# Optimization experiments

Hardware: AMD Instinct MI355X
Metric: run time of the kernel (lower is better)

The kernel has to match this reference:

```python
import jax, jax.numpy as jnp
import numpy as np

B, C_IN, H, W = 4, 1536, 64, 64   # SGI input: cat of three 512-ch encoder maps at 64x64
HID, OUT = 1536, 512
N = H * W


def _grid_edge_index(h, w):
    # 4-connected bidirectional grid, matching SGI.grid_edge_index
    idx = np.arange(h * w).reshape(h, w)
    right = np.stack([idx[:, :-1].ravel(), idx[:, 1:].ravel()])
    down = np.stack([idx[:-1, :].ravel(), idx[1:, :].ravel()])
    ei = np.concatenate([right, down, right[::-1], down[::-1]], axis=1)
    return ei.astype(np.int32)


def setup_inputs() -> dict:
    key = jax.random.key(0)
    ks = jax.random.split(key, 7)
    ei = _grid_edge_index(H, W)
    s = 0.02
    return {
        "x":  jax.random.normal(ks[0], (B, C_IN, H, W), jnp.float32),
        "W1": jax.random.normal(ks[1], (C_IN, HID), jnp.float32) * s,
        "b1": jnp.zeros((HID,), jnp.float32),
        "W2": jax.random.normal(ks[2], (HID, OUT), jnp.float32) * s,
        "b2": jnp.zeros((OUT,), jnp.float32),
        "Wl": jax.random.normal(ks[3], (C_IN, OUT), jnp.float32) * s,
        "bl": jnp.zeros((OUT,), jnp.float32),
        "src": jnp.asarray(ei[0]),
        "dst": jnp.asarray(ei[1]),
    }


def _gcn(h_in, Wt, b, src, dst, inv_sqrt_deg, inv_deg):
    # PyG GCNConv: lin -> symmetric-normalized aggregation (with self loops) -> +bias
    h = h_in @ Wt                                   # [B, N, F]
    norm = inv_sqrt_deg[src] * inv_sqrt_deg[dst]    # [E]
    msgs = h[:, src, :] * norm[None, :, None]       # [B, E, F]
    # self-loop contribution has norm 1/deg_i
    agg = (h * inv_deg[None, :, None]).at[:, dst, :].add(msgs)
    return agg + b


def reference(x, W1, b1, W2, b2, Wl, bl, src, dst):
    Bb, C, Hh, Ww = x.shape
    n = Hh * Ww
    # degree including self loop (graph is symmetric)
    deg = jnp.zeros((n,), x.dtype).at[dst].add(1.0) + 1.0
    inv_sqrt_deg = jax.lax.rsqrt(deg)
    inv_deg = 1.0 / deg

    xt = x.reshape(Bb, C, n).transpose(0, 2, 1)     # [B, N, C]
    identity = xt
    origin = xt @ Wl + bl                           # [B, N, OUT]
    h = jax.nn.relu(_gcn(xt, W1, b1, src, dst, inv_sqrt_deg, inv_deg))
    h = _gcn(h + identity, W2, b2, src, dst, inv_sqrt_deg, inv_deg)
    out = h * origin                                # [B, N, OUT]
    return out.transpose(0, 2, 1).reshape(Bb, out.shape[-1], Hh, Ww)
```

## Files before the change

### kernel.cpp

```cpp
#include <hip/hip_runtime.h>
#include <hip/hip_bf16.h>
#include <stdint.h>


typedef __bf16 bf16;
typedef float f32x4 __attribute__((ext_vector_type(4)));
typedef bf16 bf16x8 __attribute__((ext_vector_type(8)));

#define NB 4
#define NN 4096
#define CIN 1536
#define HIDF 1536
#define OUTF 512

__device__ __forceinline__ float degree_of(int n) {
  const int x = n & 63, y = n >> 6;
  return 1.0f + (x > 0) + (x < 63) + (y > 0) + (y < 63);
}
__device__ __forceinline__ float deg2(int gx, int gy) {
  return 1.0f + (gx > 0) + (gx < 63) + (gy > 0) + (gy < 63);
}

#define XBLK 6144
#define W1BLK 576
#define W2BLK 192

__global__ __launch_bounds__(256) void prep(
    const float* __restrict__ x, const float* __restrict__ W1,
    const float* __restrict__ W2, const float* __restrict__ Wl,
    bf16* __restrict__ xt, bf16* __restrict__ xa, bf16* __restrict__ w1t,
    bf16* __restrict__ w2t, bf16* __restrict__ wlt) {
  __shared__ float vt[64 * 64];
  __shared__ float at[64 * 64];
  const int B = blockIdx.x, t = threadIdx.x;
  const int tx = t & 15, ty = t >> 4;
  const int lane = t & 63, w = t >> 6;
  const int u = lane & 7, n3 = lane >> 3;

  if (B < XBLK) {
    const int slot = B >> 3;
    const int nt = (B & 7) * 8 + (slot & 7);
    const int ct = (slot >> 3) % 24;
    const int bb = (slot >> 3) / 24;
    const int gy = nt;
    const int n0 = nt * 64, c0 = ct * 64;
    const float* xb = x + (long)bb * CIN * NN;
#pragma unroll
    for (int cc = 0; cc < 4; cc++) {
      const int cl = ty * 4 + cc;
      const float* row = xb + (long)(c0 + cl) * NN + n0;
      const int nb = tx * 4;
      f32x4 v = *(const f32x4*)(row + nb);
      f32x4 up = {0.f, 0.f, 0.f, 0.f};
      f32x4 dn = {0.f, 0.f, 0.f, 0.f};
      if (gy > 0) up = *(const f32x4*)(row + nb - 64);
      if (gy < 63) dn = *(const f32x4*)(row + nb + 64);
      const float lf = (tx > 0) ? row[nb - 1] : 0.f;
      const float rt = (tx < 15) ? row[nb + 4] : 0.f;
      f32x4 a;
#pragma unroll
      for (int i = 0; i < 4; i++) {
        const int gx = nb + i;
        const float degn = deg2(gx, gy);
        float s = v[i] * (1.0f / degn);
        const float lv = (i == 0) ? lf : v[i - 1];
        const float rv = (i == 3) ? rt : v[i + 1];
        if (gx > 0) s += lv * rsqrtf(degn * deg2(gx - 1, gy));
        if (gx < 63) s += rv * rsqrtf(degn * deg2(gx + 1, gy));
        if (gy > 0) s += up[i] * rsqrtf(degn * deg2(gx, gy - 1));
        if (gy < 63) s += dn[i] * rsqrtf(degn * deg2(gx, gy + 1));
        a[i] = s;
      }
      const int chunk = tx ^ (2 * ((cl >> 3) & 7));
      *(f32x4*)&vt[cl * 64 + chunk * 4] = v;
      *(f32x4*)&at[cl * 64 + chunk * 4] = a;
    }
    __syncthreads();
    bf16* xtb = xt + (long)bb * NN * CIN;
    bf16* xab = xa + (long)bb * NN * CIN;
#pragma unroll
    for (int q = 0; q < 4; q++) {
      const int j = q * 4 + w;
      const int arr = j & 1, r = j >> 1;
      const int nl = n3 + 8 * r;
      const float* s = arr ? at : vt;
      bf16x8 o;
#pragma unroll
      for (int jj = 0; jj < 8; jj++) {
        const int cl = u * 8 + jj;
        const int col = nl ^ (8 * ((cl >> 3) & 7));
        o[jj] = (bf16)s[cl * 64 + col];
      }
      bf16* outp = arr ? xab : xtb;
      *(bf16x8*)&outp[(long)(n0 + nl) * CIN + c0 + u * 8] = o;
    }
  } else {
    int B2 = B - XBLK;
    const float* srcp;
    bf16* dstp;
    int Fdim, Kd, nt, ct;
    if (B2 < W1BLK) {
      nt = B2 / 24; ct = B2 % 24; srcp = W1; dstp = w1t; Fdim = HIDF; Kd = CIN;
    } else if (B2 < W1BLK + W2BLK) {
      const int l = B2 - W1BLK;
      nt = l / 24; ct = l % 24; srcp = W2; dstp = w2t; Fdim = OUTF; Kd = HIDF;
    } else {
      const int l = B2 - W1BLK - W2BLK;
      nt = l / 24; ct = l % 24; srcp = Wl; dstp = wlt; Fdim = OUTF; Kd = CIN;
    }
    const int n0 = nt * 64, c0 = ct * 64;
#pragma unroll
    for (int cc = 0; cc < 4; cc++) {
      const int cl = ty * 4 + cc;
      const float* row = srcp + (long)(c0 + cl) * Fdim + n0;
      f32x4 v = *(const f32x4*)(row + tx * 4);
      const int chunk = tx ^ (2 * ((cl >> 3) & 7));
      *(f32x4*)&vt[cl * 64 + chunk * 4] = v;
    }
    __syncthreads();
#pragma unroll
    for (int q = 0; q < 2; q++) {
      const int r = q * 4 + w;
      const int nl = n3 + 8 * r;
      bf16x8 o;
#pragma unroll
      for (int jj = 0; jj < 8; jj++) {
        const int cl = u * 8 + jj;
        const int col = nl ^ (8 * ((cl >> 3) & 7));
        o[jj] = (bf16)vt[cl * 64 + col];
      }
      *(bf16x8*)&dstp[(long)(n0 + nl) * Kd + c0 + u * 8] = o;
    }
  }
}

__device__ __forceinline__ void async_copy16(const void* g, void* l) {
  __builtin_amdgcn_global_load_lds(
      (const __attribute__((address_space(1))) void*)g,
      (__attribute__((address_space(3))) void*)l, 16, 0, 0);
}

struct GemmCtx {
  f32x4 acc[4][4];
  int wave, lane, wm, wn, quad, l15;
};

__device__ __forceinline__ void gemm_init(GemmCtx& cx, int t) {
  cx.wave = t >> 6;
  cx.lane = t & 63;
  cx.wm = (cx.wave & 1) * 64;
  cx.wn = (cx.wave >> 1) * 64;
  cx.quad = cx.lane >> 4;
  cx.l15 = cx.lane & 15;
#pragma unroll
  for (int i = 0; i < 4; i++)
#pragma unroll
    for (int j = 0; j < 4; j++) cx.acc[i][j] = {0.f, 0.f, 0.f, 0.f};
}

template <int K>
__device__ __forceinline__ void gemm_kloop(GemmCtx& cx, const bf16* Ab,
                                           const bf16* Bb, bf16* As,
                                           bf16* Bs) {
  const int r = cx.lane >> 3, c8 = cx.lane & 7;
  const int fchunk = c8 ^ r;
  constexpr int NT = K / 64;
#pragma unroll
  for (int i = 0; i < 4; i++) {
    const int row = i * 32 + cx.wave * 8;
    async_copy16(Ab + (long)(row + r) * K + fchunk * 8, &As[row * 64]);
    async_copy16(Bb + (long)(row + r) * K + fchunk * 8, &Bs[row * 64]);
  }
  __syncthreads();
#pragma unroll 2
  for (int t = 0; t < NT; ++t) {
    const int cur = (t & 1) * (128 * 64);
    const int nxt = cur ^ (128 * 64);
    const int ktn = ((t + 1 < NT) ? t + 1 : t) * 64;
#pragma unroll
    for (int i = 0; i < 4; i++) {
      const int row = i * 32 + cx.wave * 8;
      async_copy16(Ab + (long)(row + r) * K + ktn + fchunk * 8,
                   &As[nxt + row * 64]);
      async_copy16(Bb + (long)(row + r) * K + ktn + fchunk * 8,
                   &Bs[nxt + row * 64]);
    }
#pragma unroll
    for (int kk = 0; kk < 2; kk++) {
      const int q = kk * 4 + cx.quad;
      bf16x8 af[4], bfv[4];
#pragma unroll
      for (int mr = 0; mr < 4; mr++) {
        const int m = cx.wm + mr * 16 + cx.l15;
        af[mr] = *(const bf16x8*)&As[cur + m * 64 + (q ^ (m & 7)) * 8];
      }
#pragma unroll
      for (int nc = 0; nc < 4; nc++) {
        const int n = cx.wn + nc * 16 + cx.l15;
        bfv[nc] = *(const bf16x8*)&Bs[cur + n * 64 + (q ^ (n & 7)) * 8];
      }
#pragma unroll
      for (int mr = 0; mr < 4; mr++)
#pragma unroll
        for (int nc = 0; nc < 4; nc++)
          cx.acc[mr][nc] = __builtin_amdgcn_mfma_f32_16x16x32_bf16(
              af[mr], bfv[nc], cx.acc[mr][nc], 0, 0, 0);
    }
    __syncthreads();
  }
}

__global__ __launch_bounds__(256) void gemm_h(
    const bf16* __restrict__ xa, const bf16* __restrict__ w1t,
    const bf16* __restrict__ xt, bf16* __restrict__ h,
    const float* __restrict__ b1, int zbase) {
  __shared__ bf16 As[2 * 128 * 64];
  __shared__ bf16 Bs[2 * 128 * 64];
  GemmCtx cx;
  gemm_init(cx, threadIdx.x);
  const int m0 = blockIdx.x * 128, n0 = blockIdx.y * 128;
  const int z = blockIdx.z + zbase;
  gemm_kloop<CIN>(cx, xa + (long)z * NN * CIN + (long)m0 * CIN,
                  w1t + (long)n0 * CIN, As, Bs);
  const bf16* Xb = xt + (long)z * NN * HIDF;
  bf16* Cb = h + (long)z * NN * HIDF;
#pragma unroll
  for (int mr = 0; mr < 4; mr++)
#pragma unroll
    for (int nc = 0; nc < 4; nc++) {
      const int gn = n0 + cx.wn + nc * 16 + cx.l15;
      const float bv = b1[gn];
#pragma unroll
      for (int j = 0; j < 4; j++) {
        const int gm = m0 + cx.wm + mr * 16 + cx.quad * 4 + j;
        float v = cx.acc[mr][nc][j] + bv;
        v = v > 0.f ? v : 0.f;
        Cb[(long)gm * HIDF + gn] = (bf16)(v + (float)Xb[(long)gm * HIDF + gn]);
      }
    }
}

template <bool ADD_BIAS>
__global__ __launch_bounds__(256) void gemm_f32(
    const bf16* __restrict__ A, const bf16* __restrict__ Bw,
    float* __restrict__ C, const float* __restrict__ bias) {
  __shared__ bf16 As[2 * 128 * 64];
  __shared__ bf16 Bs[2 * 128 * 64];
  GemmCtx cx;
  gemm_init(cx, threadIdx.x);
  const int m0 = blockIdx.x * 128, n0 = blockIdx.y * 128, z = blockIdx.z;
  gemm_kloop<CIN>(cx, A + (long)z * NN * CIN + (long)m0 * CIN,
                  Bw + (long)n0 * CIN, As, Bs);
  float* Cb = C + (long)z * NN * OUTF;
#pragma unroll
  for (int mr = 0; mr < 4; mr++)
#pragma unroll
    for (int nc = 0; nc < 4; nc++) {
      const int gn = n0 + cx.wn + nc * 16 + cx.l15;
      float bv = 0.f;
      if (ADD_BIAS) bv = bias[gn];
#pragma unroll
      for (int j = 0; j < 4; j++) {
        const int gm = m0 + cx.wm + mr * 16 + cx.quad * 4 + j;
        Cb[(long)gm * OUTF + gn] = cx.acc[mr][nc][j] + bv;
      }
    }
}

__global__ __launch_bounds__(256) void stencil2(
    const float* __restrict__ G2, const float* __restrict__ Orig,
    const float* __restrict__ b2, float* __restrict__ out) {
  __shared__ float tile[16][516];
  const int blk = blockIdx.x;
  const int s = ((blk & 7) << 5) + (blk >> 3);
  const int n0 = s * 16, b = blockIdx.y;
  const int t = threadIdx.x;
  const int fq = t & 127, nl = t >> 7;
  const int f = fq * 4;
  const f32x4 bv = *(const f32x4*)(b2 + f);
#pragma unroll
  for (int p = 0; p < 8; p++) {
    const int nLoc = p * 2 + nl;
    const int n = n0 + nLoc;
    const int gx = n & 63, gy = n >> 6;
    const float degn = degree_of(n);
    const float ws = 1.0f / degn;
    const long rb = ((long)b * NN + n) * (long)OUTF + f;
    f32x4 g = *(const f32x4*)(G2 + rb);
    f32x4 a;
#pragma unroll
    for (int i = 0; i < 4; i++) a[i] = g[i] * ws;
    if (gx > 0) {
      const float w = rsqrtf(degn * degree_of(n - 1));
      f32x4 u = *(const f32x4*)(G2 + rb - OUTF);
#pragma unroll
      for (int i = 0; i < 4; i++) a[i] += u[i] * w;
    }
    if (gx < 63) {
      const float w = rsqrtf(degn * degree_of(n + 1));
      f32x4 u = *(const f32x4*)(G2 + rb + OUTF);
#pragma unroll
      for (int i = 0; i < 4; i++) a[i] += u[i] * w;
    }
    if (gy > 0) {
      const float w = rsqrtf(degn * degree_of(n - 64));
      f32x4 u = *(const f32x4*)(G2 + rb - 64L * OUTF);
#pragma unroll
      for (int i = 0; i < 4; i++) a[i] += u[i] * w;
    }
    if (gy < 63) {
      const float w = rsqrtf(degn * degree_of(n + 64));
      f32x4 u = *(const f32x4*)(G2 + rb + 64L * OUTF);
#pragma unroll
      for (int i = 0; i < 4; i++) a[i] += u[i] * w;
    }
    f32x4 og = *(const f32x4*)(Orig + rb);
    f32x4 res;
#pragma unroll
    for (int i = 0; i < 4; i++) res[i] = (a[i] + bv[i]) * og[i];
    *(f32x4*)&tile[nLoc][f] = res;
  }
  __syncthreads();
  const int j = t & 3, fr = t >> 2;
#pragma unroll
  for (int q = 0; q < 8; q++) {
    const int ff = q * 64 + fr;
    f32x4 v;
#pragma unroll
    for (int k = 0; k < 4; k++) v[k] = tile[j * 4 + k][ff];
    *(f32x4*)&out[((long)b * OUTF + ff) * (long)NN + n0 + j * 4] = v;
  }
}

extern "C" void kernel_launch(void* const* d_in, const int* in_sizes, int n_in,
                              void* d_out, int out_size, void* d_ws,
                              size_t ws_size, hipStream_t stream) {
  const float* x = (const float*)d_in[0];
  const float* W1 = (const float*)d_in[1];
  const float* b1 = (const float*)d_in[2];
  const float* W2 = (const float*)d_in[3];
  const float* b2 = (const float*)d_in[4];
  const float* Wl = (const float*)d_in[5];
  const float* bl = (const float*)d_in[6];
  float* out = (float*)d_out;

  uint8_t* ws = (uint8_t*)d_ws;
  size_t off = 0;
  auto alloc = [&](size_t bytes) -> void* {
    void* p = ws + off;
    off += (bytes + 255) & ~(size_t)255;
    return p;
  };
  bf16* xt = (bf16*)alloc((size_t)NB * NN * CIN * 2);
  bf16* xa = (bf16*)alloc((size_t)NB * NN * CIN * 2);
  bf16* hb = (bf16*)alloc((size_t)NB * NN * HIDF * 2);
  bf16* w1t = (bf16*)alloc((size_t)HIDF * CIN * 2);
  bf16* w2t = (bf16*)alloc((size_t)OUTF * HIDF * 2);
  bf16* wlt = (bf16*)alloc((size_t)OUTF * CIN * 2);
  float* origin = (float*)xa;
  float* g2 = (float*)xt;

  prep<<<XBLK + W1BLK + 2 * W2BLK, 256, 0, stream>>>(x, W1, W2, Wl, xt, xa,
                                                     w1t, w2t, wlt);
  gemm_h<<<dim3(NN / 128, HIDF / 128, 2), 256, 0, stream>>>(xa, w1t, xt, hb,
                                                            b1, 0);
  gemm_h<<<dim3(NN / 128, HIDF / 128, 2), 256, 0, stream>>>(xa, w1t, xt, hb,
                                                            b1, 2);
  gemm_f32<true><<<dim3(NN / 128, OUTF / 128, NB), 256, 0, stream>>>(
      xt, wlt, origin, bl);
  gemm_f32<false><<<dim3(NN / 128, OUTF / 128, NB), 256, 0, stream>>>(
      hb, w2t, g2, nullptr);
  stencil2<<<dim3(256, NB), 256, 0, stream>>>(g2, origin, b2, out);
}
```

Before: 386.7 us.

## Factor GCN normalization into constant rsqrt terms, shuffle halo loads, merge gemm_h launches

Replaces per-neighbour rsqrtf(deg_i*deg_j) with a factored form: each neighbour is scaled by a constant 1/sqrt(deg) looked up from the neighbour count, and the sum is multiplied once by the center's 1/sqrt(deg). This applies to both the prep stencil and stencil2. In prep, the left and right halo scalars now come from wavefront shuffles instead of extra global loads. The two half-batch gemm_h launches are merged into one launch over all batches, removing a launch and a tail. Using shuffles for the halo relies on lane adjacency matching the tx layout, and lanes at row edges get values that are then masked out.

Result: faster. 366.2 us (-5.3%).

```diff
diff --git a/kernel.cpp b/kernel.cpp
--- a/kernel.cpp
+++ b/kernel.cpp
@@ -13,12 +13,9 @@
 #define HIDF 1536
 #define OUTF 512
 
-__device__ __forceinline__ float degree_of(int n) {
-  const int x = n & 63, y = n >> 6;
-  return 1.0f + (x > 0) + (x < 63) + (y > 0) + (y < 63);
-}
-__device__ __forceinline__ float deg2(int gx, int gy) {
-  return 1.0f + (gx > 0) + (gx < 63) + (gy > 0) + (gy < 63);
+__device__ __forceinline__ float rs_of(int gx, int gy) {
+  const int d = (gx > 0) + (gx < 63) + (gy > 0) + (gy < 63);
+  return d == 2 ? 0.57735027f : (d == 3 ? 0.5f : 0.44721360f);
 }
 
 #define XBLK 6144
@@ -55,21 +52,21 @@
       f32x4 dn = {0.f, 0.f, 0.f, 0.f};
       if (gy > 0) up = *(const f32x4*)(row + nb - 64);
       if (gy < 63) dn = *(const f32x4*)(row + nb + 64);
-      const float lf = (tx > 0) ? row[nb - 1] : 0.f;
-      const float rt = (tx < 15) ? row[nb + 4] : 0.f;
+      const float lf = __shfl_up(v[3], 1);
+      const float rt = __shfl_down(v[0], 1);
       f32x4 a;
 #pragma unroll
       for (int i = 0; i < 4; i++) {
         const int gx = nb + i;
-        const float degn = deg2(gx, gy);
-        float s = v[i] * (1.0f / degn);
+        const float rs_s = rs_of(gx, gy);
         const float lv = (i == 0) ? lf : v[i - 1];
         const float rv = (i == 3) ? rt : v[i + 1];
-        if (gx > 0) s += lv * rsqrtf(degn * deg2(gx - 1, gy));
-        if (gx < 63) s += rv * rsqrtf(degn * deg2(gx + 1, gy));
-        if (gy > 0) s += up[i] * rsqrtf(degn * deg2(gx, gy - 1));
-        if (gy < 63) s += dn[i] * rsqrtf(degn * deg2(gx, gy + 1));
-        a[i] = s;
+        float sum = v[i] * rs_s;
+        if (gx > 0) sum += lv * rs_of(gx - 1, gy);
+        if (gx < 63) sum += rv * rs_of(gx + 1, gy);
+        if (gy > 0) sum += up[i] * rs_of(gx, gy - 1);
+        if (gy < 63) sum += dn[i] * rs_of(gx, gy + 1);
+        a[i] = rs_s * sum;
       }
       const int chunk = tx ^ (2 * ((cl >> 3) & 7));
       *(f32x4*)&vt[cl * 64 + chunk * 4] = v;
@@ -213,13 +210,12 @@
 __global__ __launch_bounds__(256) void gemm_h(
     const bf16* __restrict__ xa, const bf16* __restrict__ w1t,
     const bf16* __restrict__ xt, bf16* __restrict__ h,
-    const float* __restrict__ b1, int zbase) {
+    const float* __restrict__ b1) {
   __shared__ bf16 As[2 * 128 * 64];
   __shared__ bf16 Bs[2 * 128 * 64];
   GemmCtx cx;
   gemm_init(cx, threadIdx.x);
-  const int m0 = blockIdx.x * 128, n0 = blockIdx.y * 128;
-  const int z = blockIdx.z + zbase;
+  const int m0 = blockIdx.x * 128, n0 = blockIdx.y * 128, z = blockIdx.z;
   gemm_kloop<CIN>(cx, xa + (long)z * NN * CIN + (long)m0 * CIN,
                   w1t + (long)n0 * CIN, As, Bs);
   const bf16* Xb = xt + (long)z * NN * HIDF;
@@ -283,33 +279,32 @@
     const int nLoc = p * 2 + nl;
     const int n = n0 + nLoc;
     const int gx = n & 63, gy = n >> 6;
-    const float degn = degree_of(n);
-    const float ws = 1.0f / degn;
+    const float rs_n = rs_of(gx, gy);
     const long rb = ((long)b * NN + n) * (long)OUTF + f;
     f32x4 g = *(const f32x4*)(G2 + rb);
     f32x4 a;
 #pragma unroll
-    for (int i = 0; i < 4; i++) a[i] = g[i] * ws;
+    for (int i = 0; i < 4; i++) a[i] = g[i] * rs_n;
     if (gx > 0) {
-      const float w = rsqrtf(degn * degree_of(n - 1));
+      const float w = rs_of(gx - 1, gy);
       f32x4 u = *(const f32x4*)(G2 + rb - OUTF);
 #pragma unroll
       for (int i = 0; i < 4; i++) a[i] += u[i] * w;
     }
     if (gx < 63) {
-      const float w = rsqrtf(degn * degree_of(n + 1));
+      const float w = rs_of(gx + 1, gy);
       f32x4 u = *(const f32x4*)(G2 + rb + OUTF);
 #pragma unroll
       for (int i = 0; i < 4; i++) a[i] += u[i] * w;
     }
     if (gy > 0) {
-      const float w = rsqrtf(degn * degree_of(n - 64));
+      const float w = rs_of(gx, gy - 1);
       f32x4 u = *(const f32x4*)(G2 + rb - 64L * OUTF);
 #pragma unroll
       for (int i = 0; i < 4; i++) a[i] += u[i] * w;
     }
     if (gy < 63) {
-      const float w = rsqrtf(degn * degree_of(n + 64));
+      const float w = rs_of(gx, gy + 1);
       f32x4 u = *(const f32x4*)(G2 + rb + 64L * OUTF);
 #pragma unroll
       for (int i = 0; i < 4; i++) a[i] += u[i] * w;
@@ -317,7 +312,7 @@
     f32x4 og = *(const f32x4*)(Orig + rb);
     f32x4 res;
 #pragma unroll
-    for (int i = 0; i < 4; i++) res[i] = (a[i] + bv[i]) * og[i];
+    for (int i = 0; i < 4; i++) res[i] = (a[i] * rs_n + bv[i]) * og[i];
     *(f32x4*)&tile[nLoc][f] = res;
   }
   __syncthreads();
@@ -362,10 +357,8 @@
 
   prep<<<XBLK + W1BLK + 2 * W2BLK, 256, 0, stream>>>(x, W1, W2, Wl, xt, xa,
                                                      w1t, w2t, wlt);
-  gemm_h<<<dim3(NN / 128, HIDF / 128, 2), 256, 0, stream>>>(xa, w1t, xt, hb,
-                                                            b1, 0);
-  gemm_h<<<dim3(NN / 128, HIDF / 128, 2), 256, 0, stream>>>(xa, w1t, xt, hb,
-                                                            b1, 2);
+  gemm_h<<<dim3(NN / 128, HIDF / 128, NB), 256, 0, stream>>>(xa, w1t, xt, hb,
+                                                             b1);
   gemm_f32<true><<<dim3(NN / 128, OUTF / 128, NB), 256, 0, stream>>>(
       xt, wlt, origin, bl);
   gemm_f32<false><<<dim3(NN / 128, OUTF / 128, NB), 256, 0, stream>>>(
```
